# Optimization experiments

Measured on AMD Instinct MI355X. Metric: run time of the kernel, lower is better.

The kernel has to match this reference:

```python
import jax, jax.numpy as jnp
import numpy as np
from jax import lax

B, CH_G, H, W = 4, 64, 240, 320
C_FEA = 8           # must equal NUM for the 'cos' branch broadcast to work (as in the original)
NUM = 8             # k_f*k_f - 1
K_G = 3
IDX_REF = NUM // 2  # 4
AFF_GAMMA = 0.5     # aff_scale_const = gamma * num = 4.0 (TGASS)


def setup_inputs() -> dict:
    key = jax.random.key(0)
    k1, k2, k3, k4, k5 = jax.random.split(key, 5)
    guidance = jax.random.normal(k1, (B, CH_G, H, W), jnp.float32)
    gt_depth_conf = jax.random.uniform(k2, (B, 1, H, W), jnp.float32)
    tgtimg_fea = jax.random.normal(k3, (B, C_FEA, H // 2, W // 2), jnp.float32)
    # torch zero-inits these; use small random weights so offsets are nontrivial
    conv_w = jax.random.normal(k4, (3 * NUM, CH_G, K_G, K_G), jnp.float32) * 0.05
    conv_b = jax.random.normal(k5, (3 * NUM,), jnp.float32) * 0.01
    aff_scale_const = jnp.full((1,), AFF_GAMMA * NUM, jnp.float32)
    return {"guidance": guidance, "gt_depth_conf": gt_depth_conf, "tgtimg_fea": tgtimg_fea,
            "conv_w": conv_w, "conv_b": conv_b, "aff_scale_const": aff_scale_const}


def _bilinear_zeros(img, x, y):
    """img: (C,Hh,Ww); x,y: (P,) absolute pixel coords. Bilinear, zero outside (== grid_sample
    align_corners=True padding_mode='zeros' and the deformable-conv im2col sampling)."""
    C, Hh, Ww = img.shape
    x0 = jnp.floor(x)
    y0 = jnp.floor(y)
    wx = x - x0
    wy = y - y0

    def g(xi, yi):
        valid = (xi >= 0) & (xi <= Ww - 1) & (yi >= 0) & (yi <= Hh - 1)
        xc = jnp.clip(xi, 0, Ww - 1).astype(jnp.int32)
        yc = jnp.clip(yi, 0, Hh - 1).astype(jnp.int32)
        return img[:, yc, xc] * valid[None].astype(img.dtype)  # (C,P)

    return (g(x0, y0) * ((1 - wy) * (1 - wx))[None]
            + g(x0 + 1, y0) * ((1 - wy) * wx)[None]
            + g(x0, y0 + 1) * (wy * (1 - wx))[None]
            + g(x0 + 1, y0 + 1) * (wy * wx)[None])


def _forward(guidance, gt_depth_conf, tgtimg_fea, conv_w, conv_b, aff_scale_const):
    Bq, _, Hh, Ww = guidance.shape
    pad = (K_G - 1) // 2
    oa = lax.conv_general_dilated(guidance, conv_w, (1, 1), [(pad, pad), (pad, pad)])
    oa = oa + conv_b[None, :, None, None]
    o1, o2, aff = jnp.split(oa, 3, axis=1)                                  # each (B,NUM,H,W)
    offset = jnp.concatenate([o1, o2], axis=1).reshape(Bq, NUM, 2, Hh, Ww)  # faithful cat+view

    # ---- cosine affinity via grid-sampling the (detached) upsampled target features ----
    fea_up = lax.stop_gradient(jax.image.resize(tgtimg_fea, (Bq, C_FEA, Hh, Ww), "bilinear"))
    xg, yg = jnp.meshgrid(jnp.arange(Hh, dtype=jnp.float32),
                          jnp.arange(Ww, dtype=jnp.float32), indexing="ij")
    # repeat_interleave along last dim: [x]*NUM then [y]*NUM
    xy = jnp.repeat(jnp.stack([xg, yg], axis=-1), NUM, axis=-1)             # (H,W,2*NUM)
    off_perm = offset.reshape(Bq, 2 * NUM, Hh, Ww).transpose(0, 2, 3, 1)    # (B,H,W,2*NUM)
    xy_off = (off_perm + xy[None]).reshape(Bq, Hh, Ww, NUM, 2)
    # original normalizes [...,0] by (W-1) and [...,1] by (H-1); with align_corners=True
    # grid_sample exactly undoes it, so [...,0] is the x/width coord, [...,1] the y/height coord
    px = xy_off[..., 0].reshape(Bq, -1)
    py = xy_off[..., 1].reshape(Bq, -1)
    sampled = jax.vmap(_bilinear_zeros)(fea_up, px, py)                     # (B,C,H*W*NUM)
    # faithful to the original's raw reshape of the (B,C,H,W*NUM) grid_sample output
    offset_feas = sampled.reshape(Bq, Hh, Ww, NUM, C_FEA).transpose(0, 3, 1, 2, 4)  # (B,NUM,H,W,C)
    fea_rep = fea_up[..., None]                                             # (B,C,H,W,1) -> bcast NUM
    cos_w = (offset_feas * fea_rep).sum(axis=1).transpose(0, 3, 1, 2)       # (B,NUM,H,W); needs C==NUM
    aff = aff * cos_w                                                       # use_aff=True

    # insert zero reference offset at center index
    zref = jnp.zeros((Bq, 1, 2, Hh, Ww), offset.dtype)
    offset_full = jnp.concatenate([offset[:, :IDX_REF], zref, offset[:, IDX_REF:]],
                                  axis=1).reshape(Bq, -1, Hh, Ww)           # (B,2*(NUM+1),H,W)

    # TGASS scaling
    aff = jnp.tanh(aff) / (aff_scale_const + 1e-8)

    # ---- confidence propagation: 1x1 modulated deform conv with w=1, b=0, modulation=1
    # == bilinear sample of gt_depth_conf at (p + offset); offsets detached in the original ----
    off_det = lax.stop_gradient(offset)
    ii = jnp.arange(Hh, dtype=jnp.float32)[:, None]
    jj = jnp.arange(Ww, dtype=jnp.float32)[None, :]
    py2 = (off_det[:, :, 0] + ii).reshape(Bq, -1)   # channel 0 = dy
    px2 = (off_det[:, :, 1] + jj).reshape(Bq, -1)   # channel 1 = dx
    conf = jax.vmap(_bilinear_zeros)(gt_depth_conf, px2, py2).reshape(Bq, NUM, Hh, Ww)
    aff = aff * conf

    # ---- normalize and build reference affinity ----
    aff_abs_sum = jnp.abs(aff).sum(axis=1, keepdims=True) + 1e-4
    aff_abs_sum = jnp.maximum(aff_abs_sum, 1.0)     # TGASS clamp
    aff = aff / aff_abs_sum
    aff_ref = 1.0 - aff.sum(axis=1, keepdims=True)
    aff_full = jnp.concatenate([aff[:, :IDX_REF], aff_ref, aff[:, IDX_REF:]], axis=1)
    aff_full = jax.nn.softmax(aff_full, axis=1)     # (B,NUM+1,H,W)
    return offset_full, aff_full


def reference(guidance, gt_depth_conf, tgtimg_fea, conv_w, conv_b, aff_scale_const):
    return _forward(guidance, gt_depth_conf, tgtimg_fea, conv_w, conv_b, aff_scale_const)
```

## Files before the change

kernel.cpp:

```cpp
#include <hip/hip_runtime.h>
#include <hip/hip_bf16.h>

typedef __hip_bfloat16 bf16;
typedef __bf16 bf16x8 __attribute__((ext_vector_type(8)));
typedef float f32x4 __attribute__((ext_vector_type(4)));

#define BB 4
#define HH 240
#define WW 320
#define CG 64
#define NCO 24
#define HWSZ (HH*WW)

__device__ __forceinline__ float ldF(const void* __restrict__ p, long i, int isbf) {
    if (isbf) return __bfloat162float(((const bf16*)p)[i]);
    return ((const float*)p)[i];
}

__device__ __forceinline__ int detect_bf16(const void* asc) {
    return ((const unsigned short*)asc)[0] != 0;
}

__device__ __forceinline__ unsigned short f2bfbits(float v) {
    bf16 h = __float2bfloat16(v);
    return *(unsigned short*)&h;
}

__device__ __forceinline__ void ld4bf(const void* __restrict__ p, long i, int isbf,
                                      unsigned short* __restrict__ o) {
    if (isbf) {
        ushort4 v = *(const ushort4*)((const unsigned short*)p + i);
        o[0] = v.x; o[1] = v.y; o[2] = v.z; o[3] = v.w;
    } else {
        float4 v = *(const float4*)((const float*)p + i);
        o[0] = f2bfbits(v.x); o[1] = f2bfbits(v.y);
        o[2] = f2bfbits(v.z); o[3] = f2bfbits(v.w);
    }
}

__global__ __launch_bounds__(256) void upsample_kernel(const void* __restrict__ tin,
                                                       const void* __restrict__ asc,
                                                       float* __restrict__ fea) {
    int isbf = detect_bf16(asc);
    int idx = blockIdx.x * 256 + threadIdx.x;
    if (idx >= BB * 8 * HWSZ) return;
    int j = idx % WW;
    int rest = idx / WW;
    int i = rest % HH;
    int bc = rest / HH;
    float sy = 0.5f * (float)i - 0.25f;
    float sx = 0.5f * (float)j - 0.25f;
    float y0f = floorf(sy), x0f = floorf(sx);
    float wy = sy - y0f, wx = sx - x0f;
    int y0 = (int)y0f, x0 = (int)x0f;
    int y0c = min(max(y0, 0), 119), y1c = min(max(y0 + 1, 0), 119);
    int x0c = min(max(x0, 0), 159), x1c = min(max(x0 + 1, 0), 159);
    long base = (long)bc * 120 * 160;
    float v00 = ldF(tin, base + y0c * 160 + x0c, isbf);
    float v01 = ldF(tin, base + y0c * 160 + x1c, isbf);
    float v10 = ldF(tin, base + y1c * 160 + x0c, isbf);
    float v11 = ldF(tin, base + y1c * 160 + x1c, isbf);
    fea[idx] = (1.f - wy) * ((1.f - wx) * v00 + wx * v01)
             + wy * ((1.f - wx) * v10 + wx * v11);
}

__global__ __launch_bounds__(256) void tgt_cl_kernel(const void* __restrict__ tin,
                                                     const void* __restrict__ asc,
                                                     float* __restrict__ tcl) {
    int isbf = detect_bf16(asc);
    int idx = blockIdx.x * 256 + threadIdx.x;
    if (idx >= BB * 8 * 120 * 160) return;
    int x = idx % 160;
    int r = idx / 160;
    int yy = r % 120;
    int rc = r / 120;
    int ch = rc % 8;
    int b = rc / 8;
    float v = ldF(tin, idx, isbf);
    tcl[((((size_t)b * 120 + yy) * 160 + x) << 3) + ch] = v;
}

__global__ __launch_bounds__(256) void upsample_cl2_kernel(const float* __restrict__ tcl,
                                                           float* __restrict__ fea_cl) {
    int idx = blockIdx.x * 256 + threadIdx.x;
    if (idx >= BB * HWSZ) return;
    int j = idx % WW;
    int rest = idx / WW;
    int i = rest % HH;
    int b = rest / HH;
    float sy = 0.5f * (float)i - 0.25f;
    float sx = 0.5f * (float)j - 0.25f;
    float y0f = floorf(sy), x0f = floorf(sx);
    float wy = sy - y0f, wx = sx - x0f;
    int y0 = (int)y0f, x0 = (int)x0f;
    int y0c = min(max(y0, 0), 119), y1c = min(max(y0 + 1, 0), 119);
    int x0c = min(max(x0, 0), 159), x1c = min(max(x0 + 1, 0), 159);

    const float* s = tcl + ((size_t)b * 120 * 160) * 8;
    const float* p00 = s + ((size_t)y0c * 160 + x0c) * 8;
    const float* p01 = s + ((size_t)y0c * 160 + x1c) * 8;
    const float* p10 = s + ((size_t)y1c * 160 + x0c) * 8;
    const float* p11 = s + ((size_t)y1c * 160 + x1c) * 8;
    float v00[8], v01[8], v10[8], v11[8], o[8];
    *(float4*)&v00[0] = *(const float4*)p00; *(float4*)&v00[4] = *(const float4*)(p00 + 4);
    *(float4*)&v01[0] = *(const float4*)p01; *(float4*)&v01[4] = *(const float4*)(p01 + 4);
    *(float4*)&v10[0] = *(const float4*)p10; *(float4*)&v10[4] = *(const float4*)(p10 + 4);
    *(float4*)&v11[0] = *(const float4*)p11; *(float4*)&v11[4] = *(const float4*)(p11 + 4);
#pragma unroll
    for (int ch = 0; ch < 8; ch++)
        o[ch] = (1.f - wy) * ((1.f - wx) * v00[ch] + wx * v01[ch])
              + wy * ((1.f - wx) * v10[ch] + wx * v11[ch]);
    float* dst = fea_cl + (size_t)idx * 8;
    *(float4*)dst = make_float4(o[0], o[1], o[2], o[3]);
    *(float4*)(dst + 4) = make_float4(o[4], o[5], o[6], o[7]);
}

__global__ __launch_bounds__(256) void prep_guidance2(const void* __restrict__ g,
                                                      const void* __restrict__ asc,
                                                      unsigned short* __restrict__ gTu) {
    int isbf = detect_bf16(asc);
    const int x0 = blockIdx.x * 64;
    const int y  = blockIdx.y;
    const int b  = blockIdx.z;
    __shared__ unsigned int sh2[64][33];
    const int t = threadIdx.x;

#pragma unroll
    for (int it = 0; it < 2; it++) {
        int cp = it * 16 + (t >> 4);
        int xq = t & 15;
        long base0 = ((long)(b * CG + 2 * cp) * HH + y) * WW + x0 + 4 * xq;
        long base1 = base0 + (long)HH * WW;
        unsigned short lo[4], hi[4];
        ld4bf(g, base0, isbf, lo);
        ld4bf(g, base1, isbf, hi);
#pragma unroll
        for (int k = 0; k < 4; k++)
            sh2[4 * xq + k][cp] = (unsigned int)lo[k] | ((unsigned int)hi[k] << 16);
    }
    __syncthreads();

#pragma unroll
    for (int it = 0; it < 2; it++) {
        int s = it * 256 + t;
        int xg = s >> 3;
        int cb = s & 7;
        int4 v = make_int4((int)sh2[xg][cb * 4 + 0], (int)sh2[xg][cb * 4 + 1],
                           (int)sh2[xg][cb * 4 + 2], (int)sh2[xg][cb * 4 + 3]);
        *(int4*)&gTu[((((long)b * HH + y) * WW + x0 + xg) << 6) + cb * 8] = v;
    }
}

__global__ __launch_bounds__(256) void prep_weights(const void* __restrict__ w,
                                                    const void* __restrict__ asc,
                                                    unsigned short* __restrict__ Bpu) {
    int isbf = detect_bf16(asc);
    int idx = blockIdx.x * 256 + threadIdx.x;
    if (idx >= 18 * 32 * 32) return;
    int t = idx >> 10;
    int r = idx & 1023;
    int n = r >> 5;
    int k = r & 31;
    int tap = t >> 1;
    int ch = t & 1;
    float v = 0.f;
    if (n < NCO)
        v = ldF(w, ((long)n * CG + ch * 32 + k) * 9 + tap, isbf);
    Bpu[idx] = f2bfbits(v);
}

__global__ __launch_bounds__(256, 4) void conv_mfma3_kernel(const unsigned short* __restrict__ gTu,
                                                            const unsigned short* __restrict__ Bpu,
                                                            const void* __restrict__ bias,
                                                            const void* __restrict__ asc,
                                                            float* __restrict__ oa) {
    int isbf = detect_bf16(asc);
    const int x0 = blockIdx.x * 64;
    const int y0 = blockIdx.y * 4;
    const int b  = blockIdx.z;
    const int tid = threadIdx.x;

    __shared__ unsigned short shA[6 * 66 * 64];

#pragma unroll
    for (int it = 0; it < 13; it++) {
        int s = it * 256 + tid;
        if (s < 3168) {
            int row = s / 528;
            int rem = s - row * 528;
            int xi = rem >> 3;
            int blk = rem & 7;
            int y = y0 - 1 + row;
            int x = x0 - 1 + xi;
            int4 v = make_int4(0, 0, 0, 0);
            if (y >= 0 && y < HH && x >= 0 && x < WW)
                v = *(const int4*)(gTu + ((((size_t)b * HH + y) * WW + x) << 6)
                                       + ((blk ^ (xi & 7)) << 3));
            *(int4*)&shA[((row * 66 + xi) << 6) + (blk << 3)] = v;
        }
    }
    __syncthreads();

    const int wid  = tid >> 6;
    const int lane = tid & 63;
    const int m = lane & 15, quad = lane >> 4;

    f32x4 acc0[4], acc1[4];
#pragma unroll
    for (int r = 0; r < 4; r++) {
        acc0[r] = (f32x4){0.f, 0.f, 0.f, 0.f};
        acc1[r] = (f32x4){0.f, 0.f, 0.f, 0.f};
    }

#pragma unroll
    for (int tap = 0; tap < 9; tap++) {
        const int dy = tap / 3, dx = tap % 3;
        const int xi = wid * 16 + m + dx;
#pragma unroll
        for (int h = 0; h < 2; h++) {
            const int t = tap * 2 + h;
            int4 b0i = *(const int4*)(Bpu + ((t * 32 + m) * 32 + quad * 8));
            int4 b1i = *(const int4*)(Bpu + ((t * 32 + 16 + m) * 32 + quad * 8));
            bf16x8 bf0 = __builtin_bit_cast(bf16x8, b0i);
            bf16x8 bf1 = __builtin_bit_cast(bf16x8, b1i);
            const int sw = (((h * 4 + quad) ^ (xi & 7)) << 3);
#pragma unroll
            for (int r = 0; r < 4; r++) {
                int row = r + dy;
                int4 ai = *(const int4*)&shA[(((row * 66 + xi) << 6)) + sw];
                bf16x8 af = __builtin_bit_cast(bf16x8, ai);
                acc0[r] = __builtin_amdgcn_mfma_f32_16x16x32_bf16(af, bf0, acc0[r], 0, 0, 0);
                acc1[r] = __builtin_amdgcn_mfma_f32_16x16x32_bf16(af, bf1, acc1[r], 0, 0, 0);
            }
        }
    }

    const int n = m;
    const int x0w = x0 + wid * 16;
    float bias0 = ldF(bias, n, isbf);
    float bias1 = (n < 8) ? ldF(bias, 16 + n, isbf) : 0.f;
#pragma unroll
    for (int r = 0; r < 4; r++) {
        int yy = y0 + r;
#pragma unroll
        for (int rr = 0; rr < 4; rr++) {
            int px = x0w + quad * 4 + rr;
            float* dst = &oa[(((size_t)b * HH + yy) * WW + px) * NCO];
            dst[n] = acc0[r][rr] + bias0;
            if (n < 8) dst[16 + n] = acc1[r][rr] + bias1;
        }
    }
}

__global__ __launch_bounds__(256, 4) void conv_fallback(const void* __restrict__ g,
                                                        const void* __restrict__ w,
                                                        const void* __restrict__ bias,
                                                        const void* __restrict__ asc,
                                                        float* __restrict__ oa) {
    int isbf = detect_bf16(asc);
    const int b = blockIdx.z;
    const int i0 = blockIdx.y * 16;
    const int j0 = blockIdx.x * 16;
    const int tx = threadIdx.x & 15;
    const int ty = threadIdx.x >> 4;

    __shared__ float gl[8][18][20];
    __shared__ float wl[8][NCO][10];

    float acc[NCO];
#pragma unroll
    for (int c = 0; c < NCO; c++) acc[c] = ldF(bias, c, isbf);

    for (int ci0 = 0; ci0 < CG; ci0 += 8) {
        __syncthreads();
        for (int idx = threadIdx.x; idx < 8 * NCO * 9; idx += 256) {
            int t = idx % 9;
            int rest = idx / 9;
            int cc = rest & 7;
            int co = rest >> 3;
            wl[cc][co][t] = ldF(w, (long)(co * CG + ci0 + cc) * 9 + t, isbf);
        }
        for (int idx = threadIdx.x; idx < 8 * 18 * 18; idx += 256) {
            int cc = idx / 324;
            int rem = idx - cc * 324;
            int r = rem / 18;
            int c2 = rem - r * 18;
            int gi = i0 - 1 + r;
            int gj = j0 - 1 + c2;
            float v = 0.f;
            if (gi >= 0 && gi < HH && gj >= 0 && gj < WW)
                v = ldF(g, ((long)(b * CG + ci0 + cc) * HH + gi) * WW + gj, isbf);
            gl[cc][r][c2] = v;
        }
        __syncthreads();
#pragma unroll
        for (int cc = 0; cc < 8; cc++) {
            float ga[9];
#pragma unroll
            for (int dy = 0; dy < 3; dy++)
#pragma unroll
                for (int dx = 0; dx < 3; dx++)
                    ga[dy * 3 + dx] = gl[cc][ty + dy][tx + dx];
#pragma unroll 4
            for (int co = 0; co < NCO; co++) {
                float s = 0.f;
#pragma unroll
                for (int t = 0; t < 9; t++)
                    s += wl[cc][co][t] * ga[t];
                acc[co] += s;
            }
        }
    }
    int i = i0 + ty, j = j0 + tx;
    float4* p = (float4*)&oa[(((size_t)b * HH + i) * WW + j) * NCO];
#pragma unroll
    for (int q = 0; q < 6; q++)
        p[q] = make_float4(acc[4 * q], acc[4 * q + 1], acc[4 * q + 2], acc[4 * q + 3]);
}

__device__ __forceinline__ float bil_zero_f32(const float* __restrict__ img,
                                              float x, float y) {
    float x0f = floorf(x), y0f = floorf(y);
    float wx = x - x0f, wy = y - y0f;
    int x0 = (int)x0f, y0 = (int)y0f;
    int x0c = min(max(x0, 0), WW - 1), x1c = min(max(x0 + 1, 0), WW - 1);
    int y0c = min(max(y0, 0), HH - 1), y1c = min(max(y0 + 1, 0), HH - 1);
    float mx0 = (x0 == x0c) ? 1.f : 0.f;
    float mx1 = (x0 + 1 == x1c) ? 1.f : 0.f;
    float my0 = (y0 == y0c) ? 1.f : 0.f;
    float my1 = (y0 + 1 == y1c) ? 1.f : 0.f;
    const float* r0 = img + (size_t)y0c * WW;
    const float* r1 = img + (size_t)y1c * WW;
    float v00 = r0[x0c], v01 = r0[x1c], v10 = r1[x0c], v11 = r1[x1c];
    return my0 * (1.f - wy) * (mx0 * (1.f - wx) * v00 + mx1 * wx * v01)
         + my1 * wy * (mx0 * (1.f - wx) * v10 + mx1 * wx * v11);
}

__device__ __forceinline__ float bil_zero_poly(const void* __restrict__ img, long base,
                                               float x, float y, int isbf) {
    float x0f = floorf(x), y0f = floorf(y);
    float wx = x - x0f, wy = y - y0f;
    int x0 = (int)x0f, y0 = (int)y0f;
    int x0c = min(max(x0, 0), WW - 1), x1c = min(max(x0 + 1, 0), WW - 1);
    int y0c = min(max(y0, 0), HH - 1), y1c = min(max(y0 + 1, 0), HH - 1);
    float mx0 = (x0 == x0c) ? 1.f : 0.f;
    float mx1 = (x0 + 1 == x1c) ? 1.f : 0.f;
    float my0 = (y0 == y0c) ? 1.f : 0.f;
    float my1 = (y0 + 1 == y1c) ? 1.f : 0.f;
    long r0 = base + (long)y0c * WW;
    long r1 = base + (long)y1c * WW;
    float v00 = ldF(img, r0 + x0c, isbf), v01 = ldF(img, r0 + x1c, isbf);
    float v10 = ldF(img, r1 + x0c, isbf), v11 = ldF(img, r1 + x1c, isbf);
    return my0 * (1.f - wy) * (mx0 * (1.f - wx) * v00 + mx1 * wx * v01)
         + my1 * wy * (mx0 * (1.f - wx) * v10 + mx1 * wx * v11);
}

__global__ __launch_bounds__(256, 4) void cos_kernel(const float* __restrict__ oa,
                                                     const float* __restrict__ fea_cl,
                                                     float* __restrict__ cos_buf) {
    __shared__ float S_lds[64 * 65];
    const int bx = blockIdx.x;
    const int pi = blockIdx.y;
    const int b  = blockIdx.z;
    const int tid = threadIdx.x;
    const int qj_l = tid & 63;
    const int cpair = tid >> 6;
    const int qj = bx * 64 + qj_l;

    const float* feaB = fea_cl + (size_t)b * HWSZ * 8;
    const float4 ov = *(const float4*)&oa[(((size_t)b * HH + pi) * WW + qj) * NCO + 4 * cpair];

#pragma unroll
    for (int t = 0; t < 2; t++) {
        int c = 2 * cpair + t;
        float ox = (t == 0) ? ov.x : ov.z;
        float oy = (t == 0) ? ov.y : ov.w;
        float add = (c < 4) ? (float)pi : (float)qj;
        float px = ox + add, py = oy + add;

        float x0f = floorf(px), y0f = floorf(py);
        float wx = px - x0f, wy = py - y0f;
        int x0 = (int)x0f, y0 = (int)y0f;
        int x0c = min(max(x0, 0), WW - 1), x1c = min(max(x0 + 1, 0), WW - 1);
        int y0c = min(max(y0, 0), HH - 1), y1c = min(max(y0 + 1, 0), HH - 1);
        float mx0 = (x0 == x0c) ? 1.f : 0.f;
        float mx1 = (x0 + 1 == x1c) ? 1.f : 0.f;
        float my0 = (y0 == y0c) ? 1.f : 0.f;
        float my1 = (y0 + 1 == y1c) ? 1.f : 0.f;
        float aw = mx0 * (1.f - wx);
        float bw = mx1 * wx;
        float tw = my0 * (1.f - wy);
        float dw = my1 * wy;

        const float* r0 = feaB + (size_t)y0c * WW * 8;
        const float* r1 = feaB + (size_t)y1c * WW * 8;
        float v00[8], v01[8], v10[8], v11[8];
        *(float4*)&v00[0] = *(const float4*)(r0 + x0c * 8);
        *(float4*)&v00[4] = *(const float4*)(r0 + x0c * 8 + 4);
        *(float4*)&v01[0] = *(const float4*)(r0 + x1c * 8);
        *(float4*)&v01[4] = *(const float4*)(r0 + x1c * 8 + 4);
        *(float4*)&v10[0] = *(const float4*)(r1 + x0c * 8);
        *(float4*)&v10[4] = *(const float4*)(r1 + x0c * 8 + 4);
        *(float4*)&v11[0] = *(const float4*)(r1 + x1c * 8);
        *(float4*)&v11[4] = *(const float4*)(r1 + x1c * 8 + 4);

        int base = qj_l * 65 + c * 8;
#pragma unroll
        for (int ch = 0; ch < 8; ch++)
            S_lds[base + ch] = tw * (aw * v00[ch] + bw * v01[ch])
                             + dw * (aw * v10[ch] + bw * v11[ch]);
    }

    __syncthreads();

    if (tid < 64) {
        int g = tid >> 3;
        int c_img = tid & 7;
        int i = c_img * 30 + (pi >> 3);
        int j = (pi & 7) * 40 + bx * 8 + g;
        const float* fp = feaB + ((size_t)i * WW + j) * 8;
        float f[8];
        *(float4*)&f[0] = *(const float4*)fp;
        *(float4*)&f[4] = *(const float4*)(fp + 4);
        float acc[8];
#pragma unroll
        for (int c = 0; c < 8; c++) acc[c] = 0.f;
#pragma unroll
        for (int n = 0; n < 8; n++) {
            float fn = f[n];
            int rb = (8 * g + n) * 65 + c_img;
#pragma unroll
            for (int c = 0; c < 8; c++)
                acc[c] += fn * S_lds[rb + c * 8];
        }
        float* dst = cos_buf + (((size_t)b * HH + i) * WW + j) * 8;
        *(float4*)dst = make_float4(acc[0], acc[1], acc[2], acc[3]);
        *(float4*)(dst + 4) = make_float4(acc[4], acc[5], acc[6], acc[7]);
    }
}

__global__ __launch_bounds__(256, 4) void final2_kernel(const float* __restrict__ oa,
                                                        const float* __restrict__ cos_buf,
                                                        const void* __restrict__ conf_in,
                                                        const void* __restrict__ asc_p,
                                                        float* __restrict__ out) {
    int isbf = detect_bf16(asc_p);
    int idx = blockIdx.x * 256 + threadIdx.x;
    if (idx >= BB * HWSZ) return;
    int j = idx % WW;
    int rest = idx / WW;
    int i = rest % HH;
    int b = rest / HH;

    float cos_acc[8];
    {
        const float* cp = cos_buf + (size_t)idx * 8;
        float4 ca = *(const float4*)cp;
        float4 cb = *(const float4*)(cp + 4);
        cos_acc[0] = ca.x; cos_acc[1] = ca.y; cos_acc[2] = ca.z; cos_acc[3] = ca.w;
        cos_acc[4] = cb.x; cos_acc[5] = cb.y; cos_acc[6] = cb.z; cos_acc[7] = cb.w;
    }

    const float4* op = (const float4*)&oa[(((size_t)b * HH + i) * WW + j) * NCO];
    float own[24];
#pragma unroll
    for (int q = 0; q < 6; q++) {
        float4 v = op[q];
        own[4 * q] = v.x; own[4 * q + 1] = v.y; own[4 * q + 2] = v.z; own[4 * q + 3] = v.w;
    }

    float asc = ldF(asc_p, 0, isbf) + 1e-8f;
    long cbase = (long)b * HWSZ;

    float a[8];
    float ssum = 0.f;
#pragma unroll
    for (int c = 0; c < 8; c++) {
        float v = own[16 + c] * cos_acc[c];
        v = tanhf(v) / asc;
        float py2 = own[2 * c] + (float)i;
        float px2 = own[2 * c + 1] + (float)j;
        float cf = bil_zero_poly(conf_in, cbase, px2, py2, isbf);
        v *= cf;
        a[c] = v;
        ssum += fabsf(v);
    }
    ssum += 1e-4f;
    ssum = fmaxf(ssum, 1.0f);
    float inv = 1.0f / ssum;
    float asum = 0.f;
#pragma unroll
    for (int c = 0; c < 8; c++) { a[c] *= inv; asum += a[c]; }
    float aref = 1.0f - asum;

    float vals[9];
#pragma unroll
    for (int c = 0; c < 4; c++) vals[c] = a[c];
    vals[4] = aref;
#pragma unroll
    for (int c = 4; c < 8; c++) vals[c + 1] = a[c];
    float m = vals[0];
#pragma unroll
    for (int k = 1; k < 9; k++) m = fmaxf(m, vals[k]);
    float es = 0.f;
#pragma unroll
    for (int k = 0; k < 9; k++) { vals[k] = __expf(vals[k] - m); es += vals[k]; }
    float ei = 1.0f / es;

    size_t pix = (size_t)i * WW + j;
    size_t base_o = (size_t)b * 18 * HWSZ + pix;
#pragma unroll
    for (int ch = 0; ch < 18; ch++) {
        float v;
        if (ch < 8) v = own[ch];
        else if (ch < 10) v = 0.f;
        else v = own[ch - 2];
        out[base_o + (size_t)ch * HWSZ] = v;
    }
    float* aff_out = out + (size_t)BB * 18 * HWSZ;
    size_t base_a = (size_t)b * 9 * HWSZ + pix;
#pragma unroll
    for (int k = 0; k < 9; k++)
        aff_out[base_a + (size_t)k * HWSZ] = vals[k] * ei;
}

__global__ __launch_bounds__(256, 4) void final_kernel(const float* __restrict__ oa,
                                                       const float* __restrict__ fea,
                                                       const void* __restrict__ conf_in,
                                                       const void* __restrict__ asc_p,
                                                       float* __restrict__ out) {
    int isbf = detect_bf16(asc_p);
    int idx = blockIdx.x * 256 + threadIdx.x;
    if (idx >= BB * HWSZ) return;
    int j = idx % WW;
    int rest = idx / WW;
    int i = rest % HH;
    int b = rest / HH;

    const float* feaB = fea + (size_t)b * 8 * HWSZ;
    float f[8];
#pragma unroll
    for (int n = 0; n < 8; n++)
        f[n] = feaB[(size_t)n * HWSZ + (size_t)i * WW + j];

    int c_img = i / 30;
    int pi = (i % 30) * 8 + j / 40;
    int pj0 = (j % 40) * 8;
    const float* feaC = feaB + (size_t)c_img * HWSZ;

    float cos_acc[8];
#pragma unroll
    for (int c = 0; c < 8; c++) cos_acc[c] = 0.f;

#pragma unroll 1
    for (int n = 0; n < 8; n++) {
        int qj = pj0 + n;
        const float4* oq = (const float4*)&oa[(((size_t)b * HH + pi) * WW + qj) * NCO];
        float4 o0 = oq[0], o1 = oq[1], o2 = oq[2], o3 = oq[3];
        float off[16] = {o0.x, o0.y, o0.z, o0.w, o1.x, o1.y, o1.z, o1.w,
                         o2.x, o2.y, o2.z, o2.w, o3.x, o3.y, o3.z, o3.w};
        float fn = f[n];
#pragma unroll
        for (int c = 0; c < 8; c++) {
            float add = (c < 4) ? (float)pi : (float)qj;
            float px = off[2 * c] + add;
            float py = off[2 * c + 1] + add;
            cos_acc[c] += fn * bil_zero_f32(feaC, px, py);
        }
    }

    const float4* op = (const float4*)&oa[(((size_t)b * HH + i) * WW + j) * NCO];
    float own[24];
#pragma unroll
    for (int q = 0; q < 6; q++) {
        float4 v = op[q];
        own[4 * q] = v.x; own[4 * q + 1] = v.y; own[4 * q + 2] = v.z; own[4 * q + 3] = v.w;
    }

    float asc = ldF(asc_p, 0, isbf) + 1e-8f;
    long cbase = (long)b * HWSZ;

    float a[8];
    float ssum = 0.f;
#pragma unroll
    for (int c = 0; c < 8; c++) {
        float v = own[16 + c] * cos_acc[c];
        v = tanhf(v) / asc;
        float py2 = own[2 * c] + (float)i;
        float px2 = own[2 * c + 1] + (float)j;
        float cf = bil_zero_poly(conf_in, cbase, px2, py2, isbf);
        v *= cf;
        a[c] = v;
        ssum += fabsf(v);
    }
    ssum += 1e-4f;
    ssum = fmaxf(ssum, 1.0f);
    float inv = 1.0f / ssum;
    float asum = 0.f;
#pragma unroll
    for (int c = 0; c < 8; c++) { a[c] *= inv; asum += a[c]; }
    float aref = 1.0f - asum;

    float vals[9];
#pragma unroll
    for (int c = 0; c < 4; c++) vals[c] = a[c];
    vals[4] = aref;
#pragma unroll
    for (int c = 4; c < 8; c++) vals[c + 1] = a[c];
    float m = vals[0];
#pragma unroll
    for (int k = 1; k < 9; k++) m = fmaxf(m, vals[k]);
    float es = 0.f;
#pragma unroll
    for (int k = 0; k < 9; k++) { vals[k] = __expf(vals[k] - m); es += vals[k]; }
    float ei = 1.0f / es;

    size_t pix = (size_t)i * WW + j;
    size_t base_o = (size_t)b * 18 * HWSZ + pix;
#pragma unroll
    for (int ch = 0; ch < 18; ch++) {
        float v;
        if (ch < 8) v = own[ch];
        else if (ch < 10) v = 0.f;
        else v = own[ch - 2];
        out[base_o + (size_t)ch * HWSZ] = v;
    }
    float* aff_out = out + (size_t)BB * 18 * HWSZ;
    size_t base_a = (size_t)b * 9 * HWSZ + pix;
#pragma unroll
    for (int k = 0; k < 9; k++)
        aff_out[base_a + (size_t)k * HWSZ] = vals[k] * ei;
}

extern "C" void kernel_launch(void* const* d_in, const int* in_sizes, int n_in,
                              void* d_out, int out_size, void* d_ws, size_t ws_size,
                              hipStream_t stream) {
    const void* guidance = d_in[0];
    const void* gtconf   = d_in[1];
    const void* tgt      = d_in[2];
    const void* conv_w   = d_in[3];
    const void* conv_b   = d_in[4];
    const void* asc      = d_in[5];

    float* oa  = (float*)d_ws;
    float* fea = oa + (size_t)BB * HWSZ * NCO;
    float* big = fea + (size_t)BB * 8 * HWSZ;
    unsigned short* gTu = (unsigned short*)big;
    float* cosb = big;
    float* tcl  = big;
    unsigned short* Bpu = (unsigned short*)((char*)big + (size_t)39321600);
    const size_t ws_full = (size_t)29491200 + 9830400 + 39321600 + 36864;
    const size_t ws_mid  = (size_t)29491200 + 9830400 + 9830400;
    float* out = (float*)d_out;

    int n_pix = BB * HWSZ;
    int n_tgt = BB * 8 * 120 * 160;

    if (ws_size >= ws_full) {
        tgt_cl_kernel<<<(n_tgt + 255) / 256, 256, 0, stream>>>(tgt, asc, tcl);
        upsample_cl2_kernel<<<(n_pix + 255) / 256, 256, 0, stream>>>(tcl, fea);
        prep_weights<<<72, 256, 0, stream>>>(conv_w, asc, Bpu);
        dim3 pgrid(WW / 64, HH, BB);
        prep_guidance2<<<pgrid, 256, 0, stream>>>(guidance, asc, gTu);
        dim3 cgrid(WW / 64, HH / 4, BB);
        conv_mfma3_kernel<<<cgrid, 256, 0, stream>>>(gTu, Bpu, conv_b, asc, oa);
        dim3 ggrid(WW / 64, HH, BB);
        cos_kernel<<<ggrid, 256, 0, stream>>>(oa, fea, cosb);
        final2_kernel<<<(n_pix + 255) / 256, 256, 0, stream>>>(oa, cosb, gtconf, asc, out);
    } else if (ws_size >= ws_mid) {
        tgt_cl_kernel<<<(n_tgt + 255) / 256, 256, 0, stream>>>(tgt, asc, tcl);
        upsample_cl2_kernel<<<(n_pix + 255) / 256, 256, 0, stream>>>(tcl, fea);
        dim3 cgrid(WW / 16, HH / 16, BB);
        conv_fallback<<<cgrid, 256, 0, stream>>>(guidance, conv_w, conv_b, asc, oa);
        dim3 ggrid(WW / 64, HH, BB);
        cos_kernel<<<ggrid, 256, 0, stream>>>(oa, fea, cosb);
        final2_kernel<<<(n_pix + 255) / 256, 256, 0, stream>>>(oa, cosb, gtconf, asc, out);
    } else {
        int n_up = BB * 8 * HWSZ;
        upsample_kernel<<<(n_up + 255) / 256, 256, 0, stream>>>(tgt, asc, fea);
        dim3 cgrid(WW / 16, HH / 16, BB);
        conv_fallback<<<cgrid, 256, 0, stream>>>(guidance, conv_w, conv_b, asc, oa);
        final_kernel<<<(n_pix + 255) / 256, 256, 0, stream>>>(oa, fea, gtconf, asc, out);
    }
}
```

Before: 251.3 us.

## Write offset channels from conv epilogue and spread cos matmul across all threads

```diff
diff --git a/kernel.cpp b/kernel.cpp
--- a/kernel.cpp
+++ b/kernel.cpp
@@ -173,7 +173,8 @@
                                                             const unsigned short* __restrict__ Bpu,
                                                             const void* __restrict__ bias,
                                                             const void* __restrict__ asc,
-                                                            float* __restrict__ oa) {
+                                                            float* __restrict__ oa,
+                                                            float* __restrict__ out) {
     int isbf = detect_bf16(asc);
     const int x0 = blockIdx.x * 64;
     const int y0 = blockIdx.y * 4;
@@ -239,16 +240,34 @@
     const int x0w = x0 + wid * 16;
     float bias0 = ldF(bias, n, isbf);
     float bias1 = (n < 8) ? ldF(bias, 16 + n, isbf) : 0.f;
+
+    __syncthreads();
+    float* shO = (float*)shA;
 #pragma unroll
     for (int r = 0; r < 4; r++) {
         int yy = y0 + r;
 #pragma unroll
         for (int rr = 0; rr < 4; rr++) {
             int px = x0w + quad * 4 + rr;
+            float v0 = acc0[r][rr] + bias0;
             float* dst = &oa[(((size_t)b * HH + yy) * WW + px) * NCO];
-            dst[n] = acc0[r][rr] + bias0;
+            dst[n] = v0;
+            shO[(r * 16 + n) * 67 + (px - x0)] = v0;
             if (n < 8) dst[16 + n] = acc1[r][rr] + bias1;
         }
+    }
+    __syncthreads();
+
+#pragma unroll
+    for (int it = 0; it < 16; it++) {
+        int s = it * 256 + tid;
+        int px = s & 63;
+        int rest = s >> 6;
+        int nn = rest & 15;
+        int r = rest >> 4;
+        int och = (nn < 8) ? nn : nn + 2;
+        out[(((size_t)b * 18 + och) * HH + (y0 + r)) * WW + x0 + px]
+            = shO[(r * 16 + nn) * 67 + px];
     }
 }
 
@@ -413,30 +432,108 @@
 
     __syncthreads();
 
-    if (tid < 64) {
-        int g = tid >> 3;
-        int c_img = tid & 7;
+    {
+        int pix = tid >> 2;
+        int cp  = tid & 3;
+        int g = pix >> 3;
+        int c_img = pix & 7;
         int i = c_img * 30 + (pi >> 3);
         int j = (pi & 7) * 40 + bx * 8 + g;
         const float* fp = feaB + ((size_t)i * WW + j) * 8;
         float f[8];
         *(float4*)&f[0] = *(const float4*)fp;
         *(float4*)&f[4] = *(const float4*)(fp + 4);
-        float acc[8];
-#pragma unroll
-        for (int c = 0; c < 8; c++) acc[c] = 0.f;
+        float a0 = 0.f, a1 = 0.f;
+        int c0 = 2 * cp;
 #pragma unroll
         for (int n = 0; n < 8; n++) {
             float fn = f[n];
             int rb = (8 * g + n) * 65 + c_img;
-#pragma unroll
-            for (int c = 0; c < 8; c++)
-                acc[c] += fn * S_lds[rb + c * 8];
+            a0 += fn * S_lds[rb + c0 * 8];
+            a1 += fn * S_lds[rb + (c0 + 1) * 8];
         }
-        float* dst = cos_buf + (((size_t)b * HH + i) * WW + j) * 8;
-        *(float4*)dst = make_float4(acc[0], acc[1], acc[2], acc[3]);
-        *(float4*)(dst + 4) = make_float4(acc[4], acc[5], acc[6], acc[7]);
-    }
+        float* dst = cos_buf + (((size_t)b * HH + i) * WW + j) * 8 + c0;
+        *(float2*)dst = make_float2(a0, a1);
+    }
+}
+
+__global__ __launch_bounds__(256, 4) void final3_kernel(const float* __restrict__ oa,
+                                                        const float* __restrict__ cos_buf,
+                                                        const void* __restrict__ conf_in,
+                                                        const void* __restrict__ asc_p,
+                                                        float* __restrict__ out) {
+    int isbf = detect_bf16(asc_p);
+    int idx = blockIdx.x * 256 + threadIdx.x;
+    if (idx >= BB * HWSZ) return;
+    int j = idx % WW;
+    int rest = idx / WW;
+    int i = rest % HH;
+    int b = rest / HH;
+
+    float cos_acc[8];
+    {
+        const float* cp = cos_buf + (size_t)idx * 8;
+        float4 ca = *(const float4*)cp;
+        float4 cb = *(const float4*)(cp + 4);
+        cos_acc[0] = ca.x; cos_acc[1] = ca.y; cos_acc[2] = ca.z; cos_acc[3] = ca.w;
+        cos_acc[4] = cb.x; cos_acc[5] = cb.y; cos_acc[6] = cb.z; cos_acc[7] = cb.w;
+    }
+
+    const float4* op = (const float4*)&oa[(((size_t)b * HH + i) * WW + j) * NCO];
+    float own[24];
+#pragma unroll
+    for (int q = 0; q < 6; q++) {
+        float4 v = op[q];
+        own[4 * q] = v.x; own[4 * q + 1] = v.y; own[4 * q + 2] = v.z; own[4 * q + 3] = v.w;
+    }
+
+    float asc = ldF(asc_p, 0, isbf) + 1e-8f;
+    long cbase = (long)b * HWSZ;
+
+    float a[8];
+    float ssum = 0.f;
+#pragma unroll
+    for (int c = 0; c < 8; c++) {
+        float v = own[16 + c] * cos_acc[c];
+        v = tanhf(v) / asc;
+        float py2 = own[2 * c] + (float)i;
+        float px2 = own[2 * c + 1] + (float)j;
+        float cf = bil_zero_poly(conf_in, cbase, px2, py2, isbf);
+        v *= cf;
+        a[c] = v;
+        ssum += fabsf(v);
+    }
+    ssum += 1e-4f;
+    ssum = fmaxf(ssum, 1.0f);
+    float inv = 1.0f / ssum;
+    float asum = 0.f;
+#pragma unroll
+    for (int c = 0; c < 8; c++) { a[c] *= inv; asum += a[c]; }
+    float aref = 1.0f - asum;
+
+    float vals[9];
+#pragma unroll
+    for (int c = 0; c < 4; c++) vals[c] = a[c];
+    vals[4] = aref;
+#pragma unroll
+    for (int c = 4; c < 8; c++) vals[c + 1] = a[c];
+    float m = vals[0];
+#pragma unroll
+    for (int k = 1; k < 9; k++) m = fmaxf(m, vals[k]);
+    float es = 0.f;
+#pragma unroll
+    for (int k = 0; k < 9; k++) { vals[k] = __expf(vals[k] - m); es += vals[k]; }
+    float ei = 1.0f / es;
+
+    size_t pix = (size_t)i * WW + j;
+    size_t base_o = (size_t)b * 18 * HWSZ + pix;
+    out[base_o + (size_t)8 * HWSZ] = 0.f;
+    out[base_o + (size_t)9 * HWSZ] = 0.f;
+    float* aff_out = out + (size_t)BB * 18 * HWSZ;
+    size_t base_a = (size_t)b * 9 * HWSZ + pix;
+#pragma unroll
+    for (int k = 0; k < 9; k++)
+        aff_out[base_a + (size_t)k * HWSZ] = vals[k] * ei;
 }
 
 __global__ __launch_bounds__(256, 4) void final2_kernel(const float* __restrict__ oa,
@@ -663,10 +760,10 @@
         dim3 pgrid(WW / 64, HH, BB);
         prep_guidance2<<<pgrid, 256, 0, stream>>>(guidance, asc, gTu);
         dim3 cgrid(WW / 64, HH / 4, BB);
-        conv_mfma3_kernel<<<cgrid, 256, 0, stream>>>(gTu, Bpu, conv_b, asc, oa);
+        conv_mfma3_kernel<<<cgrid, 256, 0, stream>>>(gTu, Bpu, conv_b, asc, oa, out);
         dim3 ggrid(WW / 64, HH, BB);
         cos_kernel<<<ggrid, 256, 0, stream>>>(oa, fea, cosb);
-        final2_kernel<<<(n_pix + 255) / 256, 256, 0, stream>>>(oa, cosb, gtconf, asc, out);
+        final3_kernel<<<(n_pix + 255) / 256, 256, 0, stream>>>(oa, cosb, gtconf, asc, out);
     } else if (ws_size >= ws_mid) {
         tgt_cl_kernel<<<(n_tgt + 255) / 256, 256, 0, stream>>>(tgt, asc, tcl);
         upsample_cl2_kernel<<<(n_pix + 255) / 256, 256, 0, stream>>>(tcl, fea);
```

Result: faster. 236.3 us (-6.0%).
